# Optimization experiments

Measured on AMD Instinct MI355X. Metric: run time of the kernel, lower is better.

## Reference

```python
import jax, jax.numpy as jnp
import numpy as np

B, N = 2048, 256
CTX, LAT, CEMB, NF, H = 32, 64, 64, 8, 128
TDIM = 1 + 2 * NF            # 17
COND = TDIM + CEMB           # 81
DIN = LAT + COND             # 145
OUT = 14
EPS = 1e-5


def _ln(x, g, b):
    mu = jnp.mean(x, axis=-1, keepdims=True)
    var = jnp.mean((x - mu) ** 2, axis=-1, keepdims=True)
    return (x - mu) * jax.lax.rsqrt(var + EPS) * g + b


def _mlp(x, Ws, bs, Gs, Bes):
    # hidden: Linear -> LayerNorm -> tanh (dropout inactive in eval); final: Linear
    for W, b, g, be in zip(Ws[:-1], bs[:-1], Gs, Bes):
        x = jnp.tanh(_ln(x @ W + b, g, be))
    return x @ Ws[-1] + bs[-1]


def setup_inputs() -> dict:
    key = jax.random.key(0)
    ks = jax.random.split(key, 40)
    s = 0.05
    inp = {}
    # monotone time grid per trajectory in [0,1]
    inp['t'] = jnp.sort(jax.random.uniform(ks[0], (B, N, 1), dtype=jnp.float32), axis=1)
    inp['context'] = jax.random.normal(ks[1], (B, CTX), dtype=jnp.float32)
    # context encoder (Linear + tanh) and z0 encoder (Linear + tanh)
    inp['ce_w'] = jax.random.normal(ks[2], (CTX, CEMB), jnp.float32) * s
    inp['ce_b'] = jnp.zeros((CEMB,), jnp.float32)
    inp['z0_w'] = jax.random.normal(ks[3], (CEMB, LAT), jnp.float32) * s
    inp['z0_b'] = jnp.zeros((LAT,), jnp.float32)
    # dynamics MLP: DIN->H->H->H->LAT, LN on hidden layers
    dyn_dims = [DIN, H, H, H, LAT]
    for i in range(4):
        inp[f'dw{i}'] = jax.random.normal(ks[4 + i], (dyn_dims[i], dyn_dims[i + 1]), jnp.float32) * s
        inp[f'db{i}'] = jnp.zeros((dyn_dims[i + 1],), jnp.float32)
    for i in range(3):
        inp[f'dg{i}'] = jnp.ones((H,), jnp.float32)
        inp[f'dbe{i}'] = jnp.zeros((H,), jnp.float32)
    # decoder MLP: LAT->H->H->H->14, LN on hidden layers
    dec_dims = [LAT, H, H, H, OUT]
    for i in range(4):
        inp[f'ew{i}'] = jax.random.normal(ks[10 + i], (dec_dims[i], dec_dims[i + 1]), jnp.float32) * s
        inp[f'eb{i}'] = jnp.zeros((dec_dims[i + 1],), jnp.float32)
    for i in range(3):
        inp[f'eg{i}'] = jnp.ones((H,), jnp.float32)
        inp[f'ebe{i}'] = jnp.zeros((H,), jnp.float32)
    return inp


def _forward(t, context, ce_w, ce_b, z0_w, z0_b,
             dw0, db0, dw1, db1, dw2, db2, dw3, db3,
             dg0, dbe0, dg1, dbe1, dg2, dbe2,
             ew0, eb0, ew1, eb1, ew2, eb2, ew3, eb3,
             eg0, ebe0, eg1, ebe1, eg2, ebe2):
    dyn_Ws, dyn_bs = [dw0, dw1, dw2, dw3], [db0, db1, db2, db3]
    dyn_Gs, dyn_Bes = [dg0, dg1, dg2], [dbe0, dbe1, dbe2]
    dec_Ws, dec_bs = [ew0, ew1, ew2, ew3], [eb0, eb1, eb2, eb3]
    dec_Gs, dec_Bes = [eg0, eg1, eg2], [ebe0, ebe1, ebe2]

    # context embedding and latent initial state
    ctx_emb = jnp.tanh(context @ ce_w + ce_b)                  # [B, CEMB]
    z0 = jnp.tanh(ctx_emb @ z0_w + z0_b)                       # [B, LAT]

    # Fourier time embedding: [t, sin(f_k t), cos(f_k t)], f_k = 2^k * pi
    freqs = (2.0 ** jnp.arange(NF, dtype=jnp.float32)) * jnp.pi  # [NF]
    tf = t * freqs                                             # [B, N, NF]
    t_emb = jnp.concatenate([t, jnp.sin(tf), jnp.cos(tf)], axis=-1)  # [B, N, TDIM]

    ctx_rep = jnp.broadcast_to(ctx_emb[:, None, :], (t.shape[0], t.shape[1], CEMB))
    condition = jnp.concatenate([t_emb, ctx_rep], axis=-1)     # [B, N, COND]

    dt = t[:, 1:, 0] - t[:, :-1, 0]                            # [B, N-1]

    def step(z, inp):
        cond_i, dt_i = inp                                     # [B, COND], [B]
        dz = _mlp(jnp.concatenate([z, cond_i], axis=-1), dyn_Ws, dyn_bs, dyn_Gs, dyn_Bes)
        z_next = z + dt_i[:, None] * dz
        return z_next, z_next

    xs = (jnp.swapaxes(condition[:, :-1, :], 0, 1), jnp.swapaxes(dt, 0, 1))
    _, zs = jax.lax.scan(step, z0, xs)                         # [N-1, B, LAT]
    z_traj = jnp.concatenate([z0[:, None, :], jnp.swapaxes(zs, 0, 1)], axis=1)  # [B, N, LAT]

    return _mlp(z_traj, dec_Ws, dec_bs, dec_Gs, dec_Bes)       # [B, N, 14]


def reference(t, context, ce_w, ce_b, z0_w, z0_b,
              dw0, db0, dw1, db1, dw2, db2, dw3, db3,
              dg0, dbe0, dg1, dbe1, dg2, dbe2,
              ew0, eb0, ew1, eb1, ew2, eb2, ew3, eb3,
              eg0, ebe0, eg1, ebe1, eg2, ebe2):
    return _forward(t, context, ce_w, ce_b, z0_w, z0_b,
                    dw0, db0, dw1, db1, dw2, db2, dw3, db3,
                    dg0, dbe0, dg1, dbe1, dg2, dbe2,
                    ew0, eb0, ew1, eb1, ew2, eb2, ew3, eb3,
                    eg0, ebe0, eg1, ebe1, eg2, ebe2)
```

## Files before the change

kernel.cpp:

```cpp
#include <hip/hip_runtime.h>
#include <cstdint>
#include <cstddef>

#define B_ 2048
#define N_ 256

typedef unsigned short u16;
typedef unsigned int u32;
typedef __attribute__((ext_vector_type(8))) short short8;
typedef __attribute__((ext_vector_type(4))) float floatx4;

__device__ __forceinline__ u16 f2bf(float f) {
  union { float f; unsigned u; } v; v.f = f;
  unsigned u = v.u;
  return (u16)((u + 0x7FFFu + ((u >> 16) & 1u)) >> 16);
}
__device__ __forceinline__ u32 cvt_pk_bf16(float a, float b) {
  u32 r;
  asm("v_cvt_pk_bf16_f32 %0, %1, %2" : "=v"(r) : "v"(a), "v"(b));
  return r;
}
__device__ __forceinline__ float bfly16(float x) {
  auto r = __builtin_amdgcn_permlane16_swap(__float_as_int(x), __float_as_int(x), false, false);
  return __int_as_float(r[0]) + __int_as_float(r[1]);
}
__device__ __forceinline__ float bfly32(float x) {
  auto r = __builtin_amdgcn_permlane32_swap(__float_as_int(x), __float_as_int(x), false, false);
  return __int_as_float(r[0]) + __int_as_float(r[1]);
}
#define CC_ 2.885390081777927f
__device__ __forceinline__ float tanh_fast(float x) {
  float u = __builtin_amdgcn_exp2f(x * CC_);
  return fmaf(__builtin_amdgcn_rcpf(u + 1.0f), -2.0f, 1.0f);
}
__device__ __forceinline__ float tanh_arg(float x) {
  float u = __builtin_amdgcn_exp2f(x);
  return fmaf(__builtin_amdgcn_rcpf(u + 1.0f), -2.0f, 1.0f);
}
__device__ __forceinline__ float four_emb(float tv, int j) {
  if (j == 0) return tv;
  int jj = (j <= 8) ? j : j - 8;
  float sc = __int_as_float((jj + 125) << 23);
  float r = __builtin_amdgcn_fractf(tv * sc);
  return (j <= 8) ? __builtin_amdgcn_sinf(r) : __builtin_amdgcn_cosf(r);
}
__device__ __forceinline__ void bar_lgkm() {
  asm volatile("s_waitcnt lgkmcnt(0)" ::: "memory");
  __builtin_amdgcn_s_barrier();
  __builtin_amdgcn_sched_barrier(0);
}

__global__ void rlp_pack_all(const float* __restrict__ dw0, const float* __restrict__ dw1,
                             const float* __restrict__ dw2, const float* __restrict__ dw3,
                             const float* __restrict__ ew0, const float* __restrict__ ew1,
                             const float* __restrict__ ew2, const float* __restrict__ ew3,
                             u16* __restrict__ wdyn, u16* __restrict__ wdec) {
  int e = blockIdx.x * blockDim.x + threadIdx.x;
  const float* W; int K, Nc, ks, base; u16* dst;
  if (e < 20480)       { W = dw0; K = 145; Nc = 128; ks = 5; dst = wdyn;         base = 0; }
  else if (e < 36864)  { W = dw1; K = 128; Nc = 128; ks = 4; dst = wdyn + 20480; base = 20480; }
  else if (e < 53248)  { W = dw2; K = 128; Nc = 128; ks = 4; dst = wdyn + 36864; base = 36864; }
  else if (e < 61440)  { W = dw3; K = 128; Nc = 64;  ks = 4; dst = wdyn + 53248; base = 53248; }
  else if (e < 69632)  { W = ew0; K = 64;  Nc = 128; ks = 2; dst = wdec;         base = 61440; }
  else if (e < 86016)  { W = ew1; K = 128; Nc = 128; ks = 4; dst = wdec + 8192;  base = 69632; }
  else if (e < 102400) { W = ew2; K = 128; Nc = 128; ks = 4; dst = wdec + 24576; base = 86016; }
  else if (e < 104448) { W = ew3; K = 128; Nc = 14;  ks = 4; dst = wdec + 40960; base = 102400; }
  else return;
  int el = e - base;
  int j = el & 7;
  int lane = (el >> 3) & 63;
  int tt = el >> 9;
  int ksi = tt % ks;
  int nt = tt / ks;
  int col = nt * 16 + (lane & 15);
  int k = ksi * 32 + ((lane >> 4) << 3) + j;
  float v = 0.0f;
  if (k < K && col < Nc) v = W[k * Nc + col];
  dst[el] = f2bf(v);
}

template <int KS, int KSD>
__device__ __forceinline__ void mlp_layer2(
    const short8* wT0, const short8* wT1, const short8* xstat,
    floatx4 bv0, floatx4 bv1,
    floatx4 Asel, floatx4 Esel,
    const u16* src, u16* dst, float* lnbuf,
    int grpoff, int wl, int lane, int tsel, int wofs) {
  const int rrow = lane & 15;
  const int g = lane >> 4;
  const int srow = rrow & 7;
  short8 xf[KSD];
#pragma unroll
  for (int ks = 0; ks < KSD; ks++)
    xf[ks] = *reinterpret_cast<const short8*>(&src[srow * 168 + ks * 32 + g * 8]);
  floatx4 acc0 = bv0, acc1 = bv1;
#pragma unroll
  for (int ks = 0; ks < KSD; ks++) {
    acc0 = __builtin_amdgcn_mfma_f32_16x16x32_bf16(wT0[ks], xf[ks], acc0, 0, 0, 0);
    acc1 = __builtin_amdgcn_mfma_f32_16x16x32_bf16(wT1[ks], xf[ks], acc1, 0, 0, 0);
  }
#pragma unroll
  for (int ks = KSD; ks < KS; ks++) {
    acc0 = __builtin_amdgcn_mfma_f32_16x16x32_bf16(wT0[ks], xstat[ks - KSD], acc0, 0, 0, 0);
    acc1 = __builtin_amdgcn_mfma_f32_16x16x32_bf16(wT1[ks], xstat[ks - KSD], acc1, 0, 0, 0);
  }
  float s = ((acc0[0] + acc0[1]) + (acc0[2] + acc0[3]))
          + ((acc1[0] + acc1[1]) + (acc1[2] + acc1[3]));
  float q = ((acc0[0] * acc0[0] + acc0[1] * acc0[1]) + (acc0[2] * acc0[2] + acc0[3] * acc0[3]))
          + ((acc1[0] * acc1[0] + acc1[1] * acc1[1]) + (acc1[2] * acc1[2] + acc1[3] * acc1[3]));
  s = bfly32(bfly16(s));
  q = bfly32(bfly16(q));
  if (lane < 8)
    *reinterpret_cast<float2*>(&lnbuf[lane * 20 + grpoff + 2 * wl]) = make_float2(s, q);
  bar_lgkm();
  floatx4 p0 = *reinterpret_cast<const floatx4*>(&lnbuf[srow * 20 + grpoff + 0]);
  floatx4 p1 = *reinterpret_cast<const floatx4*>(&lnbuf[srow * 20 + grpoff + 4]);
  float S = (p0[0] + p0[2]) + (p1[0] + p1[2]);
  float Q = (p0[1] + p0[3]) + (p1[1] + p1[3]);
  float mean = S * 0.0078125f;
  float var = fmaf(Q, 0.0078125f, -mean * mean);
  float rs = __builtin_amdgcn_rsqf(var + 1e-5f);
  floatx4 acc = tsel ? acc1 : acc0;
  float a0 = fmaf((acc[0] - mean) * rs, Asel[0], Esel[0]);
  float a1 = fmaf((acc[1] - mean) * rs, Asel[1], Esel[1]);
  float a2 = fmaf((acc[2] - mean) * rs, Asel[2], Esel[2]);
  float a3 = fmaf((acc[3] - mean) * rs, Asel[3], Esel[3]);
  float h0 = tanh_arg(a0);
  float h1 = tanh_arg(a1);
  float h2 = tanh_arg(a2);
  float h3 = tanh_arg(a3);
  *reinterpret_cast<uint2*>(&dst[srow * 168 + wofs]) =
      make_uint2(cvt_pk_bf16(h0, h1), cvt_pk_bf16(h2, h3));
  bar_lgkm();
}

__global__ __launch_bounds__(512, 1) void rlp_fused4(
    const float* __restrict__ t,
    const u16* __restrict__ wdyn, const u16* __restrict__ wdec,
    const float* __restrict__ ctxg, const float* __restrict__ cew,
    const float* __restrict__ ceb, const float* __restrict__ z0w,
    const float* __restrict__ z0b,
    const float* __restrict__ db0, const float* __restrict__ db1,
    const float* __restrict__ db2, const float* __restrict__ db3,
    const float* __restrict__ dg0, const float* __restrict__ dbe0,
    const float* __restrict__ dg1, const float* __restrict__ dbe1,
    const float* __restrict__ dg2, const float* __restrict__ dbe2,
    const float* __restrict__ eb0, const float* __restrict__ eb1,
    const float* __restrict__ eb2, const float* __restrict__ eb3,
    const float* __restrict__ eg0, const float* __restrict__ ebe0,
    const float* __restrict__ eg1, const float* __restrict__ ebe1,
    const float* __restrict__ eg2, const float* __restrict__ ebe2,
    float* __restrict__ out) {
  __shared__ __align__(16) u16 xb[8 * 168];
  __shared__ __align__(16) u16 hdA[8 * 168];
  __shared__ __align__(16) u16 hdB[8 * 168];
  __shared__ __align__(16) u16 heA[8 * 168];
  __shared__ __align__(16) u16 heB[8 * 168];
  __shared__ __align__(16) float lnS[8 * 20];
  __shared__ __align__(16) float tl[8][260];
  __shared__ float ctxe[8][64];
  __shared__ float zbuf[8][64];

  const int tid = threadIdx.x;
  const int wv = tid >> 6;
  const int lane = tid & 63;
  const int rrow = lane & 15;
  const int g = lane >> 4;
  const int r8 = rrow & 7;
  const int wl = wv & 3;
  const bool isdyn = (wv < 4);
  const int grpoff = isdyn ? 0 : 8;
  const int gb = blockIdx.x * 8;
  const int tsel = (rrow >> 3) & 1;
  const int wofs = 32 * wl + tsel * 16 + 4 * g;
  const int c0 = 32 * wl + 4 * g;

  const float* pb1 = isdyn ? db0 : eb0;
  const float* pg1 = isdyn ? dg0 : eg0;
  const float* pe1 = isdyn ? dbe0 : ebe0;
  const float* pb2 = isdyn ? db1 : eb1;
  const float* pg2 = isdyn ? dg1 : eg1;
  const float* pe2 = isdyn ? dbe1 : ebe1;
  const float* pb3 = isdyn ? db2 : eb2;
  const float* pg3 = isdyn ? dg2 : eg2;
  const float* pe3 = isdyn ? dbe2 : ebe2;

  const floatx4 b1t0 = *(const floatx4*)&pb1[c0];
  const floatx4 b1t1 = *(const floatx4*)&pb1[c0 + 16];
  const floatx4 b2t0 = *(const floatx4*)&pb2[c0];
  const floatx4 b2t1 = *(const floatx4*)&pb2[c0 + 16];
  const floatx4 b3t0 = *(const floatx4*)&pb3[c0];
  const floatx4 b3t1 = *(const floatx4*)&pb3[c0 + 16];
#define FOLD4(p) {p[wofs] * CC_, p[wofs + 1] * CC_, p[wofs + 2] * CC_, p[wofs + 3] * CC_}
  const floatx4 A1s = FOLD4(pg1), E1s = FOLD4(pe1);
  const floatx4 A2s = FOLD4(pg2), E2s = FOLD4(pe2);
  const floatx4 A3s = FOLD4(pg3), E3s = FOLD4(pe3);
#undef FOLD4
  floatx4 b4;
  if (isdyn) {
    b4 = *(const floatx4*)&db3[16 * wl + 4 * g];
  } else {
    int cb = 4 * g;
    b4[0] = (cb + 0 < 14) ? eb3[cb + 0] : 0.0f;
    b4[1] = (cb + 1 < 14) ? eb3[cb + 1] : 0.0f;
    b4[2] = (cb + 2 < 14) ? eb3[cb + 2] : 0.0f;
    b4[3] = (cb + 3 < 14) ? eb3[cb + 3] : 0.0f;
  }

  short8 wA[13], wB[13], w4[4];
  if (isdyn) {
#pragma unroll
    for (int ks = 0; ks < 5; ks++) {
      wA[ks] = *(const short8*)(wdyn + ((size_t)((2 * wl + 0) * 5 + ks) * 64 + lane) * 8);
      wB[ks] = *(const short8*)(wdyn + ((size_t)((2 * wl + 1) * 5 + ks) * 64 + lane) * 8);
    }
#pragma unroll
    for (int ks = 0; ks < 4; ks++) {
      wA[5 + ks] = *(const short8*)(wdyn + 20480 + ((size_t)((2 * wl + 0) * 4 + ks) * 64 + lane) * 8);
      wB[5 + ks] = *(const short8*)(wdyn + 20480 + ((size_t)((2 * wl + 1) * 4 + ks) * 64 + lane) * 8);
      wA[9 + ks] = *(const short8*)(wdyn + 36864 + ((size_t)((2 * wl + 0) * 4 + ks) * 64 + lane) * 8);
      wB[9 + ks] = *(const short8*)(wdyn + 36864 + ((size_t)((2 * wl + 1) * 4 + ks) * 64 + lane) * 8);
      w4[ks] = *(const short8*)(wdyn + 53248 + ((size_t)(wl * 4 + ks) * 64 + lane) * 8);
    }
  } else {
#pragma unroll
    for (int ks = 0; ks < 2; ks++) {
      wA[ks] = *(const short8*)(wdec + ((size_t)((2 * wl + 0) * 2 + ks) * 64 + lane) * 8);
      wB[ks] = *(const short8*)(wdec + ((size_t)((2 * wl + 1) * 2 + ks) * 64 + lane) * 8);
    }
#pragma unroll
    for (int ks = 0; ks < 4; ks++) {
      wA[5 + ks] = *(const short8*)(wdec + 8192 + ((size_t)((2 * wl + 0) * 4 + ks) * 64 + lane) * 8);
      wB[5 + ks] = *(const short8*)(wdec + 8192 + ((size_t)((2 * wl + 1) * 4 + ks) * 64 + lane) * 8);
      wA[9 + ks] = *(const short8*)(wdec + 24576 + ((size_t)((2 * wl + 0) * 4 + ks) * 64 + lane) * 8);
      wB[9 + ks] = *(const short8*)(wdec + 24576 + ((size_t)((2 * wl + 1) * 4 + ks) * 64 + lane) * 8);
      w4[ks] = *(const short8*)(wdec + 40960 + ((size_t)ks * 64 + lane) * 8);
    }
  }
  u16* h0 = isdyn ? hdA : heA;
  u16* h1 = isdyn ? hdB : heB;

  for (int i = tid; i < 8 * 256; i += 512) {
    int r = i >> 8, c = i & 255;
    tl[r][c] = t[(size_t)(gb + r) * N_ + c];
  }
  for (int i = tid; i < 8 * 168 / 2; i += 512) reinterpret_cast<u32*>(&xb[0])[i] = 0;
  __syncthreads();
  {
    int b = tid >> 6, c = tid & 63;
    float s = ceb[c];
#pragma unroll
    for (int k = 0; k < 32; k++) s += ctxg[(size_t)(gb + b) * 32 + k] * cew[k * 64 + c];
    float v = tanh_fast(s);
    ctxe[b][c] = v;
    xb[b * 168 + 81 + c] = f2bf(v);
  }
  __syncthreads();
  {
    int b = tid >> 6, l = tid & 63;
    float s = z0b[l];
#pragma unroll 8
    for (int k = 0; k < 64; k++) s += ctxe[b][k] * z0w[k * 64 + l];
    zbuf[b][l] = tanh_fast(s);
  }
  if (tid < 136) {
    int b = tid / 17, j = tid - b * 17;
    xb[b * 168 + 64 + j] = f2bf(four_emb(tl[b][0], j));
  }
  __syncthreads();

  float zr0, zr1, zr2, zr3;
  {
    const floatx4 zv = *(const floatx4*)&zbuf[r8][16 * wl + 4 * g];
    zr0 = zv[0]; zr1 = zv[1]; zr2 = zv[2]; zr3 = zv[3];
    if (isdyn && rrow < 8) {
      *reinterpret_cast<uint2*>(&xb[rrow * 168 + 16 * wl + 4 * g]) =
          make_uint2(cvt_pk_bf16(zr0, zr1), cvt_pk_bf16(zr2, zr3));
    }
  }
  __syncthreads();

  short8 xs[2];
  xs[0] = *reinterpret_cast<const short8*>(&xb[r8 * 168 + 96 + g * 8]);
  xs[1] = *reinterpret_cast<const short8*>(&xb[r8 * 168 + 128 + g * 8]);

  float* po = out + ((size_t)(gb + r8) * N_) * 14 + 4 * g;

  for (int n = 0; n < N_; n++) {
    if (isdyn)
      mlp_layer2<5, 3>(wA, wB, xs, b1t0, b1t1, A1s, E1s,
                       xb, h0, lnS, grpoff, wl, lane, tsel, wofs);
    else
      mlp_layer2<2, 2>(wA, wB, nullptr, b1t0, b1t1, A1s, E1s,
                       xb, h0, lnS, grpoff, wl, lane, tsel, wofs);
    mlp_layer2<4, 4>(wA + 5, wB + 5, nullptr, b2t0, b2t1, A2s, E2s,
                     h0, h1, lnS, grpoff, wl, lane, tsel, wofs);
    mlp_layer2<4, 4>(wA + 9, wB + 9, nullptr, b3t0, b3t1, A3s, E3s,
                     h1, h0, lnS, grpoff, wl, lane, tsel, wofs);
    if (isdyn) {
      if (n < N_ - 1) {
        short8 xf4[4];
#pragma unroll
        for (int ks = 0; ks < 4; ks++)
          xf4[ks] = *reinterpret_cast<const short8*>(&h0[r8 * 168 + ks * 32 + g * 8]);
        floatx4 da = b4;
#pragma unroll
        for (int ks = 0; ks < 4; ks++)
          da = __builtin_amdgcn_mfma_f32_16x16x32_bf16(w4[ks], xf4[ks], da, 0, 0, 0);
        float dt = tl[r8][n + 1] - tl[r8][n];
        zr0 += dt * da[0]; zr1 += dt * da[1]; zr2 += dt * da[2]; zr3 += dt * da[3];
        if (rrow < 8) {
          *reinterpret_cast<uint2*>(&xb[rrow * 168 + 16 * wl + 4 * g]) =
              make_uint2(cvt_pk_bf16(zr0, zr1), cvt_pk_bf16(zr2, zr3));
        }
      }
    } else if (wv == 4) {
      short8 xf4[4];
#pragma unroll
      for (int ks = 0; ks < 4; ks++)
        xf4[ks] = *reinterpret_cast<const short8*>(&h0[r8 * 168 + ks * 32 + g * 8]);
      floatx4 da = b4;
#pragma unroll
      for (int ks = 0; ks < 4; ks++)
        da = __builtin_amdgcn_mfma_f32_16x16x32_bf16(w4[ks], xf4[ks], da, 0, 0, 0);
      if (rrow < 8) {
        float* p = po + (size_t)n * 14;
        *reinterpret_cast<float2*>(p) = make_float2(da[0], da[1]);
        if (g < 3) *reinterpret_cast<float2*>(p + 2) = make_float2(da[2], da[3]);
      }
    } else {
      int t2 = tid - 320;
      if (t2 < 136 && n < N_ - 2) {
        int b = t2 / 17, j = t2 - b * 17;
        xb[b * 168 + 64 + j] = f2bf(four_emb(tl[b][n + 1], j));
      }
    }
    bar_lgkm();
  }
}

extern "C" void kernel_launch(void* const* d_in, const int* in_sizes, int n_in,
                              void* d_out, int out_size, void* d_ws, size_t ws_size,
                              hipStream_t stream) {
  const float* t = (const float*)d_in[0];
  const float* ctx = (const float*)d_in[1];
  const float* ce_w = (const float*)d_in[2];
  const float* ce_b = (const float*)d_in[3];
  const float* z0_w = (const float*)d_in[4];
  const float* z0_b = (const float*)d_in[5];
  const float* dw0 = (const float*)d_in[6];
  const float* db0 = (const float*)d_in[7];
  const float* dw1 = (const float*)d_in[8];
  const float* db1 = (const float*)d_in[9];
  const float* dw2 = (const float*)d_in[10];
  const float* db2 = (const float*)d_in[11];
  const float* dw3 = (const float*)d_in[12];
  const float* db3 = (const float*)d_in[13];
  const float* dg0 = (const float*)d_in[14];
  const float* dbe0 = (const float*)d_in[15];
  const float* dg1 = (const float*)d_in[16];
  const float* dbe1 = (const float*)d_in[17];
  const float* dg2 = (const float*)d_in[18];
  const float* dbe2 = (const float*)d_in[19];
  const float* ew0 = (const float*)d_in[20];
  const float* eb0 = (const float*)d_in[21];
  const float* ew1 = (const float*)d_in[22];
  const float* eb1 = (const float*)d_in[23];
  const float* ew2 = (const float*)d_in[24];
  const float* eb2 = (const float*)d_in[25];
  const float* ew3 = (const float*)d_in[26];
  const float* eb3 = (const float*)d_in[27];
  const float* eg0 = (const float*)d_in[28];
  const float* ebe0 = (const float*)d_in[29];
  const float* eg1 = (const float*)d_in[30];
  const float* ebe1 = (const float*)d_in[31];
  const float* eg2 = (const float*)d_in[32];
  const float* ebe2 = (const float*)d_in[33];
  float* out = (float*)d_out;

  char* ws = (char*)d_ws;
  u16* wdyn = (u16*)(ws + 0);
  u16* wdec = (u16*)(ws + 122880);

  rlp_pack_all<<<408, 256, 0, stream>>>(dw0, dw1, dw2, dw3, ew0, ew1, ew2, ew3, wdyn, wdec);

  rlp_fused4<<<B_ / 8, 512, 0, stream>>>(t, wdyn, wdec, ctx, ce_w, ce_b, z0_w, z0_b,
      db0, db1, db2, db3, dg0, dbe0, dg1, dbe1, dg2, dbe2,
      eb0, eb1, eb2, eb3, eg0, ebe0, eg1, ebe1, eg2, ebe2, out);
}
```

Measured before the change: 473.9 us.

## Split each MLP layer across 16 waves with one output tile per wave

Doubles the block from 512 to 1024 threads so each wave computes a single 16-column MFMA tile per layer instead of two, with the dynamics and decoder groups each using 8 waves. The per-step serial MFMA chain per wave is halved, and the LayerNorm partial-sum exchange grows to 8 partials per row. The final-layer weights move from registers into shared memory to relieve register pressure, and the static conditioning operands are no longer cached in registers. In exchange it adds more waves hitting each barrier, more LDS reads per step, and duplicated small work.

```diff
diff --git a/kernel.cpp b/kernel.cpp
--- a/kernel.cpp
+++ b/kernel.cpp
@@ -79,62 +79,46 @@
   dst[el] = f2bf(v);
 }
 
-template <int KS, int KSD>
-__device__ __forceinline__ void mlp_layer2(
-    const short8* wT0, const short8* wT1, const short8* xstat,
-    floatx4 bv0, floatx4 bv1,
-    floatx4 Asel, floatx4 Esel,
+template <int KS>
+__device__ __forceinline__ void mlp_layer1t(
+    const short8* wT, floatx4 bv, float2 Ap, float2 Ep,
     const u16* src, u16* dst, float* lnbuf,
     int grpoff, int wl, int lane, int tsel, int wofs) {
   const int rrow = lane & 15;
   const int g = lane >> 4;
   const int srow = rrow & 7;
-  short8 xf[KSD];
-#pragma unroll
-  for (int ks = 0; ks < KSD; ks++)
+  short8 xf[KS];
+#pragma unroll
+  for (int ks = 0; ks < KS; ks++)
     xf[ks] = *reinterpret_cast<const short8*>(&src[srow * 168 + ks * 32 + g * 8]);
-  floatx4 acc0 = bv0, acc1 = bv1;
-#pragma unroll
-  for (int ks = 0; ks < KSD; ks++) {
-    acc0 = __builtin_amdgcn_mfma_f32_16x16x32_bf16(wT0[ks], xf[ks], acc0, 0, 0, 0);
-    acc1 = __builtin_amdgcn_mfma_f32_16x16x32_bf16(wT1[ks], xf[ks], acc1, 0, 0, 0);
-  }
-#pragma unroll
-  for (int ks = KSD; ks < KS; ks++) {
-    acc0 = __builtin_amdgcn_mfma_f32_16x16x32_bf16(wT0[ks], xstat[ks - KSD], acc0, 0, 0, 0);
-    acc1 = __builtin_amdgcn_mfma_f32_16x16x32_bf16(wT1[ks], xstat[ks - KSD], acc1, 0, 0, 0);
-  }
-  float s = ((acc0[0] + acc0[1]) + (acc0[2] + acc0[3]))
-          + ((acc1[0] + acc1[1]) + (acc1[2] + acc1[3]));
-  float q = ((acc0[0] * acc0[0] + acc0[1] * acc0[1]) + (acc0[2] * acc0[2] + acc0[3] * acc0[3]))
-          + ((acc1[0] * acc1[0] + acc1[1] * acc1[1]) + (acc1[2] * acc1[2] + acc1[3] * acc1[3]));
+  floatx4 acc = bv;
+#pragma unroll
+  for (int ks = 0; ks < KS; ks++)
+    acc = __builtin_amdgcn_mfma_f32_16x16x32_bf16(wT[ks], xf[ks], acc, 0, 0, 0);
+  float s = (acc[0] + acc[1]) + (acc[2] + acc[3]);
+  float q = (acc[0] * acc[0] + acc[1] * acc[1]) + (acc[2] * acc[2] + acc[3] * acc[3]);
   s = bfly32(bfly16(s));
   q = bfly32(bfly16(q));
   if (lane < 8)
-    *reinterpret_cast<float2*>(&lnbuf[lane * 20 + grpoff + 2 * wl]) = make_float2(s, q);
+    *reinterpret_cast<float2*>(&lnbuf[lane * 36 + grpoff + 2 * wl]) = make_float2(s, q);
   bar_lgkm();
-  floatx4 p0 = *reinterpret_cast<const floatx4*>(&lnbuf[srow * 20 + grpoff + 0]);
-  floatx4 p1 = *reinterpret_cast<const floatx4*>(&lnbuf[srow * 20 + grpoff + 4]);
-  float S = (p0[0] + p0[2]) + (p1[0] + p1[2]);
-  float Q = (p0[1] + p0[3]) + (p1[1] + p1[3]);
+  floatx4 p0 = *reinterpret_cast<const floatx4*>(&lnbuf[srow * 36 + grpoff + 0]);
+  floatx4 p1 = *reinterpret_cast<const floatx4*>(&lnbuf[srow * 36 + grpoff + 4]);
+  floatx4 p2 = *reinterpret_cast<const floatx4*>(&lnbuf[srow * 36 + grpoff + 8]);
+  floatx4 p3 = *reinterpret_cast<const floatx4*>(&lnbuf[srow * 36 + grpoff + 12]);
+  float S = ((p0[0] + p0[2]) + (p1[0] + p1[2])) + ((p2[0] + p2[2]) + (p3[0] + p3[2]));
+  float Q = ((p0[1] + p0[3]) + (p1[1] + p1[3])) + ((p2[1] + p2[3]) + (p3[1] + p3[3]));
   float mean = S * 0.0078125f;
-  float var = fmaf(Q, 0.0078125f, -mean * mean);
-  float rs = __builtin_amdgcn_rsqf(var + 1e-5f);
-  floatx4 acc = tsel ? acc1 : acc0;
-  float a0 = fmaf((acc[0] - mean) * rs, Asel[0], Esel[0]);
-  float a1 = fmaf((acc[1] - mean) * rs, Asel[1], Esel[1]);
-  float a2 = fmaf((acc[2] - mean) * rs, Asel[2], Esel[2]);
-  float a3 = fmaf((acc[3] - mean) * rs, Asel[3], Esel[3]);
-  float h0 = tanh_arg(a0);
-  float h1 = tanh_arg(a1);
-  float h2 = tanh_arg(a2);
-  float h3 = tanh_arg(a3);
-  *reinterpret_cast<uint2*>(&dst[srow * 168 + wofs]) =
-      make_uint2(cvt_pk_bf16(h0, h1), cvt_pk_bf16(h2, h3));
+  float rs = __builtin_amdgcn_rsqf(fmaf(Q, 0.0078125f, -mean * mean) + 1e-5f);
+  float v0 = tsel ? acc[2] : acc[0];
+  float v1 = tsel ? acc[3] : acc[1];
+  float a0 = fmaf((v0 - mean) * rs, Ap.x, Ep.x);
+  float a1 = fmaf((v1 - mean) * rs, Ap.y, Ep.y);
+  *reinterpret_cast<u32*>(&dst[srow * 168 + wofs]) = cvt_pk_bf16(tanh_arg(a0), tanh_arg(a1));
   bar_lgkm();
 }
 
-__global__ __launch_bounds__(512, 1) void rlp_fused4(
+__global__ __launch_bounds__(1024, 1) void rlp_fused5(
     const float* __restrict__ t,
     const u16* __restrict__ wdyn, const u16* __restrict__ wdec,
     const float* __restrict__ ctxg, const float* __restrict__ cew,
@@ -156,8 +140,10 @@
   __shared__ __align__(16) u16 hdB[8 * 168];
   __shared__ __align__(16) u16 heA[8 * 168];
   __shared__ __align__(16) u16 heB[8 * 168];
-  __shared__ __align__(16) float lnS[8 * 20];
+  __shared__ __align__(16) float lnS[8 * 36];
   __shared__ __align__(16) float tl[8][260];
+  __shared__ __align__(16) u16 w4d[8192];
+  __shared__ __align__(16) u16 w4e[2048];
   __shared__ float ctxe[8][64];
   __shared__ float zbuf[8][64];
 
@@ -167,13 +153,13 @@
   const int rrow = lane & 15;
   const int g = lane >> 4;
   const int r8 = rrow & 7;
-  const int wl = wv & 3;
-  const bool isdyn = (wv < 4);
-  const int grpoff = isdyn ? 0 : 8;
+  const int tsel = rrow >> 3;
+  const int wl = wv & 7;
+  const bool isdyn = (wv < 8);
+  const int grpoff = isdyn ? 0 : 16;
   const int gb = blockIdx.x * 8;
-  const int tsel = (rrow >> 3) & 1;
-  const int wofs = 32 * wl + tsel * 16 + 4 * g;
-  const int c0 = 32 * wl + 4 * g;
+  const int c0 = 16 * wl + 4 * g;
+  const int wofs = c0 + 2 * tsel;
 
   const float* pb1 = isdyn ? db0 : eb0;
   const float* pg1 = isdyn ? dg0 : eg0;
@@ -185,21 +171,19 @@
   const float* pg3 = isdyn ? dg2 : eg2;
   const float* pe3 = isdyn ? dbe2 : ebe2;
 
-  const floatx4 b1t0 = *(const floatx4*)&pb1[c0];
-  const floatx4 b1t1 = *(const floatx4*)&pb1[c0 + 16];
-  const floatx4 b2t0 = *(const floatx4*)&pb2[c0];
-  const floatx4 b2t1 = *(const floatx4*)&pb2[c0 + 16];
-  const floatx4 b3t0 = *(const floatx4*)&pb3[c0];
-  const floatx4 b3t1 = *(const floatx4*)&pb3[c0 + 16];
-#define FOLD4(p) {p[wofs] * CC_, p[wofs + 1] * CC_, p[wofs + 2] * CC_, p[wofs + 3] * CC_}
-  const floatx4 A1s = FOLD4(pg1), E1s = FOLD4(pe1);
-  const floatx4 A2s = FOLD4(pg2), E2s = FOLD4(pe2);
-  const floatx4 A3s = FOLD4(pg3), E3s = FOLD4(pe3);
-#undef FOLD4
-  floatx4 b4;
+  const floatx4 b1 = *(const floatx4*)&pb1[c0];
+  const floatx4 b2 = *(const floatx4*)&pb2[c0];
+  const floatx4 b3 = *(const floatx4*)&pb3[c0];
+  const float2 A1 = make_float2(pg1[wofs] * CC_, pg1[wofs + 1] * CC_);
+  const float2 E1 = make_float2(pe1[wofs] * CC_, pe1[wofs + 1] * CC_);
+  const float2 A2 = make_float2(pg2[wofs] * CC_, pg2[wofs + 1] * CC_);
+  const float2 E2 = make_float2(pe2[wofs] * CC_, pe2[wofs + 1] * CC_);
+  const float2 A3 = make_float2(pg3[wofs] * CC_, pg3[wofs + 1] * CC_);
+  const float2 E3 = make_float2(pe3[wofs] * CC_, pe3[wofs + 1] * CC_);
+  floatx4 b4 = {0.0f, 0.0f, 0.0f, 0.0f};
   if (isdyn) {
-    b4 = *(const floatx4*)&db3[16 * wl + 4 * g];
-  } else {
+    if (wl < 4) b4 = *(const floatx4*)&db3[16 * wl + 4 * g];
+  } else if (wv == 8) {
     int cb = 4 * g;
     b4[0] = (cb + 0 < 14) ? eb3[cb + 0] : 0.0f;
     b4[1] = (cb + 1 < 14) ? eb3[cb + 1] : 0.0f;
@@ -207,46 +191,41 @@
     b4[3] = (cb + 3 < 14) ? eb3[cb + 3] : 0.0f;
   }
 
-  short8 wA[13], wB[13], w4[4];
+  short8 wA[13];
   if (isdyn) {
 #pragma unroll
-    for (int ks = 0; ks < 5; ks++) {
-      wA[ks] = *(const short8*)(wdyn + ((size_t)((2 * wl + 0) * 5 + ks) * 64 + lane) * 8);
-      wB[ks] = *(const short8*)(wdyn + ((size_t)((2 * wl + 1) * 5 + ks) * 64 + lane) * 8);
-    }
+    for (int ks = 0; ks < 5; ks++)
+      wA[ks] = *(const short8*)(wdyn + ((size_t)(wl * 5 + ks) * 64 + lane) * 8);
 #pragma unroll
     for (int ks = 0; ks < 4; ks++) {
-      wA[5 + ks] = *(const short8*)(wdyn + 20480 + ((size_t)((2 * wl + 0) * 4 + ks) * 64 + lane) * 8);
-      wB[5 + ks] = *(const short8*)(wdyn + 20480 + ((size_t)((2 * wl + 1) * 4 + ks) * 64 + lane) * 8);
-      wA[9 + ks] = *(const short8*)(wdyn + 36864 + ((size_t)((2 * wl + 0) * 4 + ks) * 64 + lane) * 8);
-      wB[9 + ks] = *(const short8*)(wdyn + 36864 + ((size_t)((2 * wl + 1) * 4 + ks) * 64 + lane) * 8);
-      w4[ks] = *(const short8*)(wdyn + 53248 + ((size_t)(wl * 4 + ks) * 64 + lane) * 8);
+      wA[5 + ks] = *(const short8*)(wdyn + 20480 + ((size_t)(wl * 4 + ks) * 64 + lane) * 8);
+      wA[9 + ks] = *(const short8*)(wdyn + 36864 + ((size_t)(wl * 4 + ks) * 64 + lane) * 8);
     }
   } else {
 #pragma unroll
-    for (int ks = 0; ks < 2; ks++) {
-      wA[ks] = *(const short8*)(wdec + ((size_t)((2 * wl + 0) * 2 + ks) * 64 + lane) * 8);
-      wB[ks] = *(const short8*)(wdec + ((size_t)((2 * wl + 1) * 2 + ks) * 64 + lane) * 8);
-    }
+    for (int ks = 0; ks < 2; ks++)
+      wA[ks] = *(const short8*)(wdec + ((size_t)(wl * 2 + ks) * 64 + lane) * 8);
+    wA[2] = wA[0]; wA[3] = wA[0]; wA[4] = wA[0];
 #pragma unroll
     for (int ks = 0; ks < 4; ks++) {
-      wA[5 + ks] = *(const short8*)(wdec + 8192 + ((size_t)((2 * wl + 0) * 4 + ks) * 64 + lane) * 8);
-      wB[5 + ks] = *(const short8*)(wdec + 8192 + ((size_t)((2 * wl + 1) * 4 + ks) * 64 + lane) * 8);
-      wA[9 + ks] = *(const short8*)(wdec + 24576 + ((size_t)((2 * wl + 0) * 4 + ks) * 64 + lane) * 8);
-      wB[9 + ks] = *(const short8*)(wdec + 24576 + ((size_t)((2 * wl + 1) * 4 + ks) * 64 + lane) * 8);
-      w4[ks] = *(const short8*)(wdec + 40960 + ((size_t)ks * 64 + lane) * 8);
+      wA[5 + ks] = *(const short8*)(wdec + 8192 + ((size_t)(wl * 4 + ks) * 64 + lane) * 8);
+      wA[9 + ks] = *(const short8*)(wdec + 24576 + ((size_t)(wl * 4 + ks) * 64 + lane) * 8);
     }
   }
   u16* h0 = isdyn ? hdA : heA;
   u16* h1 = isdyn ? hdB : heB;
 
-  for (int i = tid; i < 8 * 256; i += 512) {
+  for (int i = tid; i < 8 * 256; i += 1024) {
     int r = i >> 8, c = i & 255;
     tl[r][c] = t[(size_t)(gb + r) * N_ + c];
   }
-  for (int i = tid; i < 8 * 168 / 2; i += 512) reinterpret_cast<u32*>(&xb[0])[i] = 0;
+  for (int i = tid; i < 8192 / 8; i += 1024)
+    reinterpret_cast<uint4*>(w4d)[i] = reinterpret_cast<const uint4*>(wdyn + 53248)[i];
+  for (int i = tid; i < 2048 / 8; i += 1024)
+    reinterpret_cast<uint4*>(w4e)[i] = reinterpret_cast<const uint4*>(wdec + 40960)[i];
+  for (int i = tid; i < 8 * 168 / 2; i += 1024) reinterpret_cast<u32*>(&xb[0])[i] = 0;
   __syncthreads();
-  {
+  if (tid < 512) {
     int b = tid >> 6, c = tid & 63;
     float s = ceb[c];
 #pragma unroll
@@ -256,7 +235,7 @@
     xb[b * 168 + 81 + c] = f2bf(v);
   }
   __syncthreads();
-  {
+  if (tid < 512) {
     int b = tid >> 6, l = tid & 63;
     float s = z0b[l];
 #pragma unroll 8
@@ -269,44 +248,38 @@
   }
   __syncthreads();
 
-  float zr0, zr1, zr2, zr3;
-  {
+  float zr0 = 0.0f, zr1 = 0.0f, zr2 = 0.0f, zr3 = 0.0f;
+  if (isdyn && wl < 4) {
     const floatx4 zv = *(const floatx4*)&zbuf[r8][16 * wl + 4 * g];
     zr0 = zv[0]; zr1 = zv[1]; zr2 = zv[2]; zr3 = zv[3];
-    if (isdyn && rrow < 8) {
+    if (rrow < 8) {
       *reinterpret_cast<uint2*>(&xb[rrow * 168 + 16 * wl + 4 * g]) =
           make_uint2(cvt_pk_bf16(zr0, zr1), cvt_pk_bf16(zr2, zr3));
     }
   }
   __syncthreads();
 
-  short8 xs[2];
-  xs[0] = *reinterpret_cast<const short8*>(&xb[r8 * 168 + 96 + g * 8]);
-  xs[1] = *reinterpret_cast<const short8*>(&xb[r8 * 168 + 128 + g * 8]);
-
   float* po = out + ((size_t)(gb + r8) * N_) * 14 + 4 * g;
 
   for (int n = 0; n < N_; n++) {
     if (isdyn)
-      mlp_layer2<5, 3>(wA, wB, xs, b1t0, b1t1, A1s, E1s,
-                       xb, h0, lnS, grpoff, wl, lane, tsel, wofs);
+      mlp_layer1t<5>(wA, b1, A1, E1, xb, h0, lnS, grpoff, wl, lane, tsel, wofs);
     else
-      mlp_layer2<2, 2>(wA, wB, nullptr, b1t0, b1t1, A1s, E1s,
-                       xb, h0, lnS, grpoff, wl, lane, tsel, wofs);
-    mlp_layer2<4, 4>(wA + 5, wB + 5, nullptr, b2t0, b2t1, A2s, E2s,
-                     h0, h1, lnS, grpoff, wl, lane, tsel, wofs);
-    mlp_layer2<4, 4>(wA + 9, wB + 9, nullptr, b3t0, b3t1, A3s, E3s,
-                     h1, h0, lnS, grpoff, wl, lane, tsel, wofs);
+      mlp_layer1t<2>(wA, b1, A1, E1, xb, h0, lnS, grpoff, wl, lane, tsel, wofs);
+    mlp_layer1t<4>(wA + 5, b2, A2, E2, h0, h1, lnS, grpoff, wl, lane, tsel, wofs);
+    mlp_layer1t<4>(wA + 9, b3, A3, E3, h1, h0, lnS, grpoff, wl, lane, tsel, wofs);
     if (isdyn) {
-      if (n < N_ - 1) {
-        short8 xf4[4];
+      if (wl < 4 && n < N_ - 1) {
+        short8 xf4[4], w4t[4];
+#pragma unroll
+        for (int ks = 0; ks < 4; ks++) {
+          xf4[ks] = *reinterpret_cast<const short8*>(&h0[r8 * 168 + ks * 32 + g * 8]);
+          w4t[ks] = *reinterpret_cast<const short8*>(&w4d[((size_t)(wl * 4 + ks) * 64 + lane) * 8]);
+        }
+        floatx4 da = b4;
 #pragma unroll
         for (int ks = 0; ks < 4; ks++)
-          xf4[ks] = *reinterpret_cast<const short8*>(&h0[r8 * 168 + ks * 32 + g * 8]);
-        floatx4 da = b4;
-#pragma unroll
-        for (int ks = 0; ks < 4; ks++)
-          da = __builtin_amdgcn_mfma_f32_16x16x32_bf16(w4[ks], xf4[ks], da, 0, 0, 0);
+          da = __builtin_amdgcn_mfma_f32_16x16x32_bf16(w4t[ks], xf4[ks], da, 0, 0, 0);
         float dt = tl[r8][n + 1] - tl[r8][n];
         zr0 += dt * da[0]; zr1 += dt * da[1]; zr2 += dt * da[2]; zr3 += dt * da[3];
         if (rrow < 8) {
@@ -314,22 +287,24 @@
               make_uint2(cvt_pk_bf16(zr0, zr1), cvt_pk_bf16(zr2, zr3));
         }
       }
-    } else if (wv == 4) {
-      short8 xf4[4];
+    } else if (wv == 8) {
+      short8 xf4[4], w4t[4];
+#pragma unroll
+      for (int ks = 0; ks < 4; ks++) {
+        xf4[ks] = *reinterpret_cast<const short8*>(&h0[r8 * 168 + ks * 32 + g * 8]);
+        w4t[ks] = *reinterpret_cast<const short8*>(&w4e[((size_t)ks * 64 + lane) * 8]);
+      }
+      floatx4 da = b4;
 #pragma unroll
       for (int ks = 0; ks < 4; ks++)
-        xf4[ks] = *reinterpret_cast<const short8*>(&h0[r8 * 168 + ks * 32 + g * 8]);
-      floatx4 da = b4;
-#pragma unroll
-      for (int ks = 0; ks < 4; ks++)
-        da = __builtin_amdgcn_mfma_f32_16x16x32_bf16(w4[ks], xf4[ks], da, 0, 0, 0);
+        da = __builtin_amdgcn_mfma_f32_16x16x32_bf16(w4t[ks], xf4[ks], da, 0, 0, 0);
       if (rrow < 8) {
         float* p = po + (size_t)n * 14;
         *reinterpret_cast<float2*>(p) = make_float2(da[0], da[1]);
         if (g < 3) *reinterpret_cast<float2*>(p + 2) = make_float2(da[2], da[3]);
       }
-    } else {
-      int t2 = tid - 320;
+    } else if (wv >= 12) {
+      int t2 = tid - 768;
       if (t2 < 136 && n < N_ - 2) {
         int b = t2 / 17, j = t2 - b * 17;
         xb[b * 168 + 64 + j] = f2bf(four_emb(tl[b][n + 1], j));
@@ -384,7 +359,7 @@
 
   rlp_pack_all<<<408, 256, 0, stream>>>(dw0, dw1, dw2, dw3, ew0, ew1, ew2, ew3, wdyn, wdec);
 
-  rlp_fused4<<<B_ / 8, 512, 0, stream>>>(t, wdyn, wdec, ctx, ce_w, ce_b, z0_w, z0_b,
+  rlp_fused5<<<B_ / 8, 1024, 0, stream>>>(t, wdyn, wdec, ctx, ce_w, ce_b, z0_w, z0_b,
       db0, db1, db2, db3, dg0, dbe0, dg1, dbe1, dg2, dbe2,
       eb0, eb1, eb2, eb3, eg0, ebe0, eg1, ebe1, eg2, ebe2, out);
 }
```

Measured after the change: 748.5 us. +58.0%, slower.
